# Kernel optimization log

Measured on AMD Instinct MI355X. Metric: run time of the kernel, lower is better.

## Reference

```python
import jax, jax.numpy as jnp
import numpy as np

B, N, C, H = 128, 8732, 512, 19  # batch, priors, channels, feature map side
IMG = 300.0
FG = 19


def setup_inputs() -> dict:
    key = jax.random.key(0)
    ks = jax.random.split(key, 10)
    loc = jax.random.normal(ks[0], (B, N, 4), jnp.float32) * 0.5
    conf = jax.random.normal(ks[1], (B, N, 2), jnp.float32)
    priors = jax.random.uniform(ks[2], (N, 4), jnp.float32, minval=0.05, maxval=0.95)
    features = jax.random.normal(ks[3], (B, C, H, H), jnp.float32)
    w1 = jax.random.normal(ks[4], (C, 4096), jnp.float32) * 0.01
    b1 = jnp.zeros((4096,), jnp.float32)
    w2 = jax.random.normal(ks[5], (4096, 4096), jnp.float32) * 0.01
    b2 = jnp.zeros((4096,), jnp.float32)
    w3 = jax.random.normal(ks[6], (4096, FG), jnp.float32) * 0.01
    b3 = jnp.zeros((FG,), jnp.float32)
    return {"loc": loc, "conf": conf, "priors": priors, "features": features,
            "w1": w1, "b1": b1, "w2": w2, "b2": b2, "w3": w3, "b3": b3}


def _decode(loc, priors):
    # SSD decode, variances=[0.1, 0.2]; priors are (cx, cy, w, h)
    cxcy = priors[:, :2] + loc[..., :2] * 0.1 * priors[:, 2:]
    wh = priors[:, 2:] * jnp.exp(loc[..., 2:] * 0.2)
    xy1 = cxcy - 0.5 * wh
    return jnp.concatenate([xy1, xy1 + wh], axis=-1)  # [B,N,4] corner form


def _best_prior(loc, conf, priors):
    boxes = _decode(loc, priors)                       # [B,N,4]
    probs = jax.nn.softmax(conf, axis=-1)              # [B,N,2]
    car = jnp.argmax(probs, axis=-1) == 1              # [B,N] argmax class == car
    score = jnp.where(car, probs[..., 1], -jnp.inf)
    best = jnp.argmax(score, axis=-1)                  # [B]
    best_box = jnp.take_along_axis(boxes, best[:, None, None], axis=1)[:, 0]  # [B,4]
    has_car = jnp.any(car, axis=-1)                    # [B]
    geom = (best_box[:, 2] > best_box[:, 0]) & (best_box[:, 3] > best_box[:, 1])
    valid = has_car & geom
    result = jnp.where(has_car[:, None], best_box, 0.0)
    result = jnp.clip(result, 0.0, 1.0)
    return result, valid


def _extract(features, boxes, valid):
    # per-box crop + global max pool -> [B,C], zero for invalid boxes
    ceil_num = features.shape[2]
    step = IMG / ceil_num
    b = jnp.clip(boxes * IMG, 0.0, IMG) / step
    b = jnp.floor(jnp.clip(b, 0.0, ceil_num - 1.0)).astype(jnp.int32)  # [B,4]=x1,y1,x2,y2
    r = jnp.arange(ceil_num)
    mh = (r[None, :] >= b[:, 1:2]) & (r[None, :] <= b[:, 3:4])  # [B,H] rows
    mw = (r[None, :] >= b[:, 0:1]) & (r[None, :] <= b[:, 2:3])  # [B,W] cols
    mask = mh[:, None, :, None] & mw[:, None, None, :]          # [B,1,H,W]
    m = jnp.max(jnp.where(mask, features, -jnp.inf), axis=(2, 3))  # [B,C]
    return jnp.where(valid[:, None], m, 0.0)


def reference(loc, conf, priors, features, w1, b1, w2, b2, w3, b3):
    boxes, valid = _best_prior(loc, conf, priors)
    feat = _extract(features, boxes, valid)             # [B,512]
    h = jax.nn.relu(feat @ w1 + b1)
    h = jax.nn.relu(h @ w2 + b2)
    fg_cls = h @ w3 + b3                                # [B,19]
    return fg_cls, boxes, valid.astype(jnp.int32)
```

## Files before the change

### kernel.cpp

```cpp
#include <hip/hip_runtime.h>
#include <math.h>

#define BATCH 128
#define NPRI  8732
#define CCH   512
#define HH    19
#define NHID  4096
#define FGC   19

typedef unsigned short u16;
typedef __attribute__((ext_vector_type(8))) short bf16x8;
typedef __attribute__((ext_vector_type(4))) float f32x4;

__device__ __forceinline__ u16 f2bf(float f) {
  unsigned u = __float_as_uint(f);
  u += 0x7fff + ((u >> 16) & 1);
  return (u16)(u >> 16);
}

__global__ void k_best(const float* __restrict__ conf,
                       const float* __restrict__ loc,
                       const float* __restrict__ priors,
                       float* __restrict__ out_boxes,
                       float* __restrict__ out_valid,
                       int4* __restrict__ crop, int* __restrict__ vflag) {
  int b = blockIdx.x;
  int t = threadIdx.x;
  const float4* cb = (const float4*)(conf + (size_t)b * NPRI * 2);
  float bd = -INFINITY; int bn = 0x7fffffff;
  for (int j = t; j < NPRI / 2; j += 256) {
    float4 v = cb[j];
    float d0 = v.y - v.x, d1 = v.w - v.z;
    if (d0 > bd) { bd = d0; bn = 2 * j; }
    if (d1 > bd) { bd = d1; bn = 2 * j + 1; }
  }
  __shared__ float ls[256]; __shared__ int li[256];
  ls[t] = bd; li[t] = bn;
  __syncthreads();
  for (int off = 128; off > 0; off >>= 1) {
    if (t < off) {
      float s2 = ls[t + off]; int n2 = li[t + off];
      if (s2 > ls[t] || (s2 == ls[t] && n2 < li[t])) { ls[t] = s2; li[t] = n2; }
    }
    __syncthreads();
  }
  if (t == 0) {
    float bdf = ls[0]; int bnf = li[0];
    bool hc = bdf > 0.0f;
    float r0 = 0.f, r1 = 0.f, r2 = 0.f, r3 = 0.f;
    bool valid = false;
    if (hc) {
      const float* lp = loc + ((size_t)b * NPRI + bnf) * 4;
      const float* pp = priors + (size_t)bnf * 4;
      float l0 = lp[0], l1 = lp[1], l2 = lp[2], l3 = lp[3];
      float pcx = pp[0], pcy = pp[1], pw = pp[2], ph = pp[3];
      float cx = pcx + (l0 * 0.1f) * pw;
      float cy = pcy + (l1 * 0.1f) * ph;
      float w = pw * expf(l2 * 0.2f);
      float h = ph * expf(l3 * 0.2f);
      float x1 = cx - 0.5f * w, y1 = cy - 0.5f * h;
      float x2 = x1 + w, y2 = y1 + h;
      valid = (x2 > x1) && (y2 > y1);
      r0 = fminf(fmaxf(x1, 0.f), 1.f);
      r1 = fminf(fmaxf(y1, 0.f), 1.f);
      r2 = fminf(fmaxf(x2, 0.f), 1.f);
      r3 = fminf(fmaxf(y2, 0.f), 1.f);
    }
    out_boxes[b * 4 + 0] = r0; out_boxes[b * 4 + 1] = r1;
    out_boxes[b * 4 + 2] = r2; out_boxes[b * 4 + 3] = r3;
    out_valid[b] = valid ? 1.0f : 0.0f;
    const float stepF = (float)(300.0 / 19.0);
    float q0 = fminf(fmaxf(r0 * 300.0f, 0.0f), 300.0f) / stepF;
    float q1 = fminf(fmaxf(r1 * 300.0f, 0.0f), 300.0f) / stepF;
    float q2 = fminf(fmaxf(r2 * 300.0f, 0.0f), 300.0f) / stepF;
    float q3 = fminf(fmaxf(r3 * 300.0f, 0.0f), 300.0f) / stepF;
    int ix1 = (int)floorf(fminf(fmaxf(q0, 0.0f), 18.0f));
    int iy1 = (int)floorf(fminf(fmaxf(q1, 0.0f), 18.0f));
    int ix2 = (int)floorf(fminf(fmaxf(q2, 0.0f), 18.0f));
    int iy2 = (int)floorf(fminf(fmaxf(q3, 0.0f), 18.0f));
    crop[b] = make_int4(ix1, iy1, ix2, iy2);
    vflag[b] = valid ? 1 : 0;
  }
}

__global__ void k_extract(const float* __restrict__ fin,
                          const int4* __restrict__ crop,
                          const int* __restrict__ vflag,
                          u16* __restrict__ feat) {
  int blk = blockIdx.x;
  int b = blk >> 7;
  int tile = blk & 127;
  int wave = threadIdx.x >> 6;
  int lane = threadIdx.x & 63;
  int c = tile * 4 + wave;
  if (!vflag[b]) {
    if (lane == 0) feat[b * CCH + c] = 0;
    return;
  }
  int4 cr = crop[b];
  const float* p = fin + (size_t)(b * CCH + c) * (HH * HH);
  float m = -INFINITY;
  #pragma unroll
  for (int it = 0; it < 6; it++) {
    int idx = it * 64 + lane;
    if (idx < HH * HH) {
      int yy = idx / HH, xx = idx - yy * HH;
      bool in = (yy >= cr.y) & (yy <= cr.w) & (xx >= cr.x) & (xx <= cr.z);
      float v = p[idx];
      if (in) m = fmaxf(m, v);
    }
  }
  #pragma unroll
  for (int off = 32; off > 0; off >>= 1) m = fmaxf(m, __shfl_xor(m, off));
  if (lane == 0) feat[b * CCH + c] = f2bf(m);
}

__global__ __launch_bounds__(256) void k_gemm1(const u16* __restrict__ A,
                                               const float* __restrict__ W,
                                               const float* __restrict__ bias,
                                               u16* __restrict__ H1) {
  const int N = NHID, K = CCH;
  int nb = blockIdx.x;
  int t = threadIdx.x;
  int lane = t & 63, wave = t >> 6;
  int q = lane >> 4, r = lane & 15;
  int wm = (wave & 1) * 64, wn = (wave >> 1) * 32;
  int n0 = nb * 64;

  __shared__ u16 As[128 * 40];
  __shared__ u16 Bs[64 * 40];

  f32x4 acc[4][2];
  #pragma unroll
  for (int i = 0; i < 4; i++)
    #pragma unroll
    for (int j = 0; j < 2; j++) {
      acc[i][j].x = 0.f; acc[i][j].y = 0.f; acc[i][j].z = 0.f; acc[i][j].w = 0.f;
    }

  int am = t >> 1, ah = (t & 1) * 16;
  int kp = t >> 4;
  int n4 = (t & 15) * 4;

  for (int k0 = 0; k0 < K; k0 += 32) {
    const u16* asrc = A + (size_t)am * K + k0 + ah;
    uint4 a0 = *(const uint4*)asrc;
    uint4 a1 = *(const uint4*)(asrc + 8);
    const float* wsrc = W + (size_t)(k0 + 2 * kp) * N + n0 + n4;
    float4 w0 = *(const float4*)wsrc;
    float4 w1v = *(const float4*)(wsrc + N);
    __syncthreads();
    *(uint4*)&As[am * 40 + ah]     = a0;
    *(uint4*)&As[am * 40 + ah + 8] = a1;
    {
      unsigned pk0 = (unsigned)f2bf(w0.x) | ((unsigned)f2bf(w1v.x) << 16);
      unsigned pk1 = (unsigned)f2bf(w0.y) | ((unsigned)f2bf(w1v.y) << 16);
      unsigned pk2 = (unsigned)f2bf(w0.z) | ((unsigned)f2bf(w1v.z) << 16);
      unsigned pk3 = (unsigned)f2bf(w0.w) | ((unsigned)f2bf(w1v.w) << 16);
      *(unsigned*)&Bs[(n4 + 0) * 40 + 2 * kp] = pk0;
      *(unsigned*)&Bs[(n4 + 1) * 40 + 2 * kp] = pk1;
      *(unsigned*)&Bs[(n4 + 2) * 40 + 2 * kp] = pk2;
      *(unsigned*)&Bs[(n4 + 3) * 40 + 2 * kp] = pk3;
    }
    __syncthreads();
    bf16x8 af[4], bfr[2];
    #pragma unroll
    for (int i = 0; i < 4; i++)
      af[i] = *(const bf16x8*)&As[(wm + 16 * i + r) * 40 + q * 8];
    #pragma unroll
    for (int j = 0; j < 2; j++)
      bfr[j] = *(const bf16x8*)&Bs[(wn + 16 * j + r) * 40 + q * 8];
    #pragma unroll
    for (int i = 0; i < 4; i++)
      #pragma unroll
      for (int j = 0; j < 2; j++)
        acc[i][j] = __builtin_amdgcn_mfma_f32_16x16x32_bf16(af[i], bfr[j],
                                                            acc[i][j], 0, 0, 0);
  }

  #pragma unroll
  for (int j = 0; j < 2; j++) {
    int col = n0 + wn + 16 * j + r;
    float bv = bias[col];
    #pragma unroll
    for (int i = 0; i < 4; i++) {
      #pragma unroll
      for (int reg = 0; reg < 4; reg++) {
        int row = wm + 16 * i + q * 4 + reg;
        float v = fmaxf(acc[i][j][reg] + bv, 0.0f);
        H1[(size_t)row * N + col] = f2bf(v);
      }
    }
  }
}

template <int KSPL>
__global__ __launch_bounds__(256) void k_mfma(const u16* __restrict__ A,
                                              const float* __restrict__ W,
                                              float* __restrict__ part, int K) {
  const int N = NHID;
  int nb = blockIdx.x;
  int ks = blockIdx.y;
  int Kper = K / KSPL;
  int k0b = ks * Kper;
  int t = threadIdx.x;
  int lane = t & 63, wave = t >> 6;
  int q = lane >> 4, r = lane & 15;

  __shared__ u16 As[128 * 40];
  __shared__ u16 Bs[64 * 40];

  int wm = (wave & 1) * 64;
  int wn = (wave >> 1) * 32;
  int n0 = nb * 64;

  f32x4 acc[4][2];
  #pragma unroll
  for (int i = 0; i < 4; i++)
    #pragma unroll
    for (int j = 0; j < 2; j++) {
      acc[i][j].x = 0.f; acc[i][j].y = 0.f; acc[i][j].z = 0.f; acc[i][j].w = 0.f;
    }

  int am = t >> 1, ah = (t & 1) * 16;
  int kp = t >> 4;
  int n4 = (t & 15) * 4;

  for (int k0 = k0b; k0 < k0b + Kper; k0 += 32) {
    const u16* asrc = A + (size_t)am * K + k0 + ah;
    uint4 a0 = *(const uint4*)asrc;
    uint4 a1 = *(const uint4*)(asrc + 8);
    const float* wsrc = W + (size_t)(k0 + 2 * kp) * N + n0 + n4;
    float4 w0 = *(const float4*)wsrc;
    float4 w1v = *(const float4*)(wsrc + N);
    __syncthreads();
    *(uint4*)&As[am * 40 + ah]     = a0;
    *(uint4*)&As[am * 40 + ah + 8] = a1;
    {
      unsigned pk0 = (unsigned)f2bf(w0.x) | ((unsigned)f2bf(w1v.x) << 16);
      unsigned pk1 = (unsigned)f2bf(w0.y) | ((unsigned)f2bf(w1v.y) << 16);
      unsigned pk2 = (unsigned)f2bf(w0.z) | ((unsigned)f2bf(w1v.z) << 16);
      unsigned pk3 = (unsigned)f2bf(w0.w) | ((unsigned)f2bf(w1v.w) << 16);
      *(unsigned*)&Bs[(n4 + 0) * 40 + 2 * kp] = pk0;
      *(unsigned*)&Bs[(n4 + 1) * 40 + 2 * kp] = pk1;
      *(unsigned*)&Bs[(n4 + 2) * 40 + 2 * kp] = pk2;
      *(unsigned*)&Bs[(n4 + 3) * 40 + 2 * kp] = pk3;
    }
    __syncthreads();
    bf16x8 af[4], bfr[2];
    #pragma unroll
    for (int i = 0; i < 4; i++)
      af[i] = *(const bf16x8*)&As[(wm + 16 * i + r) * 40 + q * 8];
    #pragma unroll
    for (int j = 0; j < 2; j++)
      bfr[j] = *(const bf16x8*)&Bs[(wn + 16 * j + r) * 40 + q * 8];
    #pragma unroll
    for (int i = 0; i < 4; i++)
      #pragma unroll
      for (int j = 0; j < 2; j++)
        acc[i][j] = __builtin_amdgcn_mfma_f32_16x16x32_bf16(af[i], bfr[j],
                                                            acc[i][j], 0, 0, 0);
  }

  float* dst = part + (size_t)ks * (BATCH * NHID);
  #pragma unroll
  for (int i = 0; i < 4; i++)
    #pragma unroll
    for (int j = 0; j < 2; j++) {
      int col = n0 + wn + 16 * j + r;
      #pragma unroll
      for (int reg = 0; reg < 4; reg++) {
        int row = wm + 16 * i + q * 4 + reg;
        dst[(size_t)row * N + col] = acc[i][j][reg];
      }
    }
}

template <int KSPL>
__global__ void k_finalize(const float* __restrict__ part,
                           const float* __restrict__ bias,
                           float* __restrict__ outf) {
  int idx = (blockIdx.x * 256 + threadIdx.x) * 4;
  float4 s = *(const float4*)(part + idx);
  #pragma unroll
  for (int p = 1; p < KSPL; p++) {
    float4 v = *(const float4*)(part + (size_t)p * (BATCH * NHID) + idx);
    s.x += v.x; s.y += v.y; s.z += v.z; s.w += v.w;
  }
  float4 bv = *(const float4*)(bias + (idx & (NHID - 1)));
  s.x = fmaxf(s.x + bv.x, 0.0f); s.y = fmaxf(s.y + bv.y, 0.0f);
  s.z = fmaxf(s.z + bv.z, 0.0f); s.w = fmaxf(s.w + bv.w, 0.0f);
  *(float4*)(outf + idx) = s;
}

__global__ void k_gemm3p(const float* __restrict__ h2,
                         const float* __restrict__ w3,
                         float* __restrict__ part3) {
  int kc = blockIdx.x;
  int t = threadIdx.x;
  __shared__ float wl[32 * FGC];
  for (int i = t; i < 32 * FGC; i += 128) wl[i] = w3[kc * 32 * FGC + i];
  __syncthreads();
  const float* hp = h2 + (size_t)t * NHID + kc * 32;
  float acc[FGC];
  #pragma unroll
  for (int j = 0; j < FGC; j++) acc[j] = 0.0f;
  for (int k = 0; k < 32; k++) {
    float hv = hp[k];
    const float* wp = &wl[k * FGC];
    #pragma unroll
    for (int j = 0; j < FGC; j++) acc[j] += hv * wp[j];
  }
  float* dst = part3 + (size_t)kc * (BATCH * FGC) + t * FGC;
  #pragma unroll
  for (int j = 0; j < FGC; j++) dst[j] = acc[j];
}

__global__ void k_fin3(const float* __restrict__ part3,
                       const float* __restrict__ b3,
                       float* __restrict__ out) {
  int j = blockIdx.x * 256 + threadIdx.x;
  if (j >= BATCH * FGC) return;
  float s = 0.0f;
  for (int p = 0; p < 128; p++) s += part3[(size_t)p * (BATCH * FGC) + j];
  out[j] = s + b3[j % FGC];
}

extern "C" void kernel_launch(void* const* d_in, const int* in_sizes, int n_in,
                              void* d_out, int out_size, void* d_ws, size_t ws_size,
                              hipStream_t stream) {
  const float* loc      = (const float*)d_in[0];
  const float* conf     = (const float*)d_in[1];
  const float* priors   = (const float*)d_in[2];
  const float* features = (const float*)d_in[3];
  const float* w1 = (const float*)d_in[4];
  const float* b1 = (const float*)d_in[5];
  const float* w2 = (const float*)d_in[6];
  const float* b2 = (const float*)d_in[7];
  const float* w3 = (const float*)d_in[8];
  const float* b3 = (const float*)d_in[9];
  float* out = (float*)d_out;

  char* ws = (char*)d_ws;
  float* part  = (float*)ws;
  float* part3 = (float*)(ws + (size_t)16 * 1024 * 1024);
  float* h2    = (float*)(ws + (size_t)18 * 1024 * 1024);
  u16*   featb = (u16*)(ws + (size_t)20 * 1024 * 1024);
  u16*   h1b   = (u16*)(ws + (size_t)20 * 1024 * 1024 + 256 * 1024);
  int4*  crop  = (int4*)(ws + (size_t)21 * 1024 * 1024 + 512 * 1024);
  int*   vfl   = (int*)(crop + BATCH);

  k_best<<<BATCH, 256, 0, stream>>>(conf, loc, priors,
                                    out + BATCH * FGC,
                                    out + BATCH * FGC + BATCH * 4, crop, vfl);
  k_extract<<<BATCH * (CCH / 4), 256, 0, stream>>>(features, crop, vfl, featb);
  k_gemm1<<<64, 256, 0, stream>>>(featb, w1, b1, h1b);
  k_mfma<8><<<dim3(64, 8), 256, 0, stream>>>(h1b, w2, part, NHID);
  k_finalize<8><<<512, 256, 0, stream>>>(part, b2, h2);
  k_gemm3p<<<128, 128, 0, stream>>>(h2, w3, part3);
  k_fin3<<<10, 256, 0, stream>>>(part3, b3, out);
}
```

Measured before the change: 275.1 us.

## Split-K first GEMM, fuse layer-2 finalize into layer-3, crop-only extract loop

```diff
diff --git a/kernel.cpp b/kernel.cpp
--- a/kernel.cpp
+++ b/kernel.cpp
@@ -1,4 +1,5 @@
 #include <hip/hip_runtime.h>
+#include <hip/hip_bf16.h>
 #include <math.h>
 
 #define BATCH 128
@@ -98,100 +99,18 @@
     return;
   }
   int4 cr = crop[b];
+  int wcnt = cr.z - cr.x + 1;
+  int cnt = wcnt * (cr.w - cr.y + 1);
   const float* p = fin + (size_t)(b * CCH + c) * (HH * HH);
   float m = -INFINITY;
-  #pragma unroll
-  for (int it = 0; it < 6; it++) {
-    int idx = it * 64 + lane;
-    if (idx < HH * HH) {
-      int yy = idx / HH, xx = idx - yy * HH;
-      bool in = (yy >= cr.y) & (yy <= cr.w) & (xx >= cr.x) & (xx <= cr.z);
-      float v = p[idx];
-      if (in) m = fmaxf(m, v);
-    }
+  for (int i = lane; i < cnt; i += 64) {
+    int yy = cr.y + i / wcnt;
+    int xx = cr.x + i % wcnt;
+    m = fmaxf(m, p[yy * HH + xx]);
   }
   #pragma unroll
   for (int off = 32; off > 0; off >>= 1) m = fmaxf(m, __shfl_xor(m, off));
   if (lane == 0) feat[b * CCH + c] = f2bf(m);
-}
-
-__global__ __launch_bounds__(256) void k_gemm1(const u16* __restrict__ A,
-                                               const float* __restrict__ W,
-                                               const float* __restrict__ bias,
-                                               u16* __restrict__ H1) {
-  const int N = NHID, K = CCH;
-  int nb = blockIdx.x;
-  int t = threadIdx.x;
-  int lane = t & 63, wave = t >> 6;
-  int q = lane >> 4, r = lane & 15;
-  int wm = (wave & 1) * 64, wn = (wave >> 1) * 32;
-  int n0 = nb * 64;
-
-  __shared__ u16 As[128 * 40];
-  __shared__ u16 Bs[64 * 40];
-
-  f32x4 acc[4][2];
-  #pragma unroll
-  for (int i = 0; i < 4; i++)
-    #pragma unroll
-    for (int j = 0; j < 2; j++) {
-      acc[i][j].x = 0.f; acc[i][j].y = 0.f; acc[i][j].z = 0.f; acc[i][j].w = 0.f;
-    }
-
-  int am = t >> 1, ah = (t & 1) * 16;
-  int kp = t >> 4;
-  int n4 = (t & 15) * 4;
-
-  for (int k0 = 0; k0 < K; k0 += 32) {
-    const u16* asrc = A + (size_t)am * K + k0 + ah;
-    uint4 a0 = *(const uint4*)asrc;
-    uint4 a1 = *(const uint4*)(asrc + 8);
-    const float* wsrc = W + (size_t)(k0 + 2 * kp) * N + n0 + n4;
-    float4 w0 = *(const float4*)wsrc;
-    float4 w1v = *(const float4*)(wsrc + N);
-    __syncthreads();
-    *(uint4*)&As[am * 40 + ah]     = a0;
-    *(uint4*)&As[am * 40 + ah + 8] = a1;
-    {
-      unsigned pk0 = (unsigned)f2bf(w0.x) | ((unsigned)f2bf(w1v.x) << 16);
-      unsigned pk1 = (unsigned)f2bf(w0.y) | ((unsigned)f2bf(w1v.y) << 16);
-      unsigned pk2 = (unsigned)f2bf(w0.z) | ((unsigned)f2bf(w1v.z) << 16);
-      unsigned pk3 = (unsigned)f2bf(w0.w) | ((unsigned)f2bf(w1v.w) << 16);
-      *(unsigned*)&Bs[(n4 + 0) * 40 + 2 * kp] = pk0;
-      *(unsigned*)&Bs[(n4 + 1) * 40 + 2 * kp] = pk1;
-      *(unsigned*)&Bs[(n4 + 2) * 40 + 2 * kp] = pk2;
-      *(unsigned*)&Bs[(n4 + 3) * 40 + 2 * kp] = pk3;
-    }
-    __syncthreads();
-    bf16x8 af[4], bfr[2];
-    #pragma unroll
-    for (int i = 0; i < 4; i++)
-      af[i] = *(const bf16x8*)&As[(wm + 16 * i + r) * 40 + q * 8];
-    #pragma unroll
-    for (int j = 0; j < 2; j++)
-      bfr[j] = *(const bf16x8*)&Bs[(wn + 16 * j + r) * 40 + q * 8];
-    #pragma unroll
-    for (int i = 0; i < 4; i++)
-      #pragma unroll
-      for (int j = 0; j < 2; j++)
-        acc[i][j] = __builtin_amdgcn_mfma_f32_16x16x32_bf16(af[i], bfr[j],
-                                                            acc[i][j], 0, 0, 0);
-  }
-
-  #pragma unroll
-  for (int j = 0; j < 2; j++) {
-    int col = n0 + wn + 16 * j + r;
-    float bv = bias[col];
-    #pragma unroll
-    for (int i = 0; i < 4; i++) {
-      #pragma unroll
-      for (int reg = 0; reg < 4; reg++) {
-        int row = wm + 16 * i + q * 4 + reg;
-        float v = fmaxf(acc[i][j][reg] + bv, 0.0f);
-        H1[(size_t)row * N + col] = f2bf(v);
-      }
-    }
-  }
 }
 
 template <int KSPL>
@@ -237,14 +156,14 @@
     *(uint4*)&As[am * 40 + ah]     = a0;
     *(uint4*)&As[am * 40 + ah + 8] = a1;
     {
-      unsigned pk0 = (unsigned)f2bf(w0.x) | ((unsigned)f2bf(w1v.x) << 16);
-      unsigned pk1 = (unsigned)f2bf(w0.y) | ((unsigned)f2bf(w1v.y) << 16);
-      unsigned pk2 = (unsigned)f2bf(w0.z) | ((unsigned)f2bf(w1v.z) << 16);
-      unsigned pk3 = (unsigned)f2bf(w0.w) | ((unsigned)f2bf(w1v.w) << 16);
-      *(unsigned*)&Bs[(n4 + 0) * 40 + 2 * kp] = pk0;
-      *(unsigned*)&Bs[(n4 + 1) * 40 + 2 * kp] = pk1;
-      *(unsigned*)&Bs[(n4 + 2) * 40 + 2 * kp] = pk2;
-      *(unsigned*)&Bs[(n4 + 3) * 40 + 2 * kp] = pk3;
+      __hip_bfloat162 p0 = __float22bfloat162_rn(make_float2(w0.x, w1v.x));
+      __hip_bfloat162 p1 = __float22bfloat162_rn(make_float2(w0.y, w1v.y));
+      __hip_bfloat162 p2 = __float22bfloat162_rn(make_float2(w0.z, w1v.z));
+      __hip_bfloat162 p3 = __float22bfloat162_rn(make_float2(w0.w, w1v.w));
+      *(__hip_bfloat162*)&Bs[(n4 + 0) * 40 + 2 * kp] = p0;
+      *(__hip_bfloat162*)&Bs[(n4 + 1) * 40 + 2 * kp] = p1;
+      *(__hip_bfloat162*)&Bs[(n4 + 2) * 40 + 2 * kp] = p2;
+      *(__hip_bfloat162*)&Bs[(n4 + 3) * 40 + 2 * kp] = p3;
     }
     __syncthreads();
     bf16x8 af[4], bfr[2];
@@ -277,9 +196,9 @@
 }
 
 template <int KSPL>
-__global__ void k_finalize(const float* __restrict__ part,
-                           const float* __restrict__ bias,
-                           float* __restrict__ outf) {
+__global__ void k_finalize_bf16(const float* __restrict__ part,
+                                const float* __restrict__ bias,
+                                u16* __restrict__ outb) {
   int idx = (blockIdx.x * 256 + threadIdx.x) * 4;
   float4 s = *(const float4*)(part + idx);
   #pragma unroll
@@ -290,21 +209,35 @@
   float4 bv = *(const float4*)(bias + (idx & (NHID - 1)));
   s.x = fmaxf(s.x + bv.x, 0.0f); s.y = fmaxf(s.y + bv.y, 0.0f);
   s.z = fmaxf(s.z + bv.z, 0.0f); s.w = fmaxf(s.w + bv.w, 0.0f);
-  *(float4*)(outf + idx) = s;
-}
-
-__global__ void k_gemm3p(const float* __restrict__ h2,
+  ushort4 o;
+  o.x = f2bf(s.x); o.y = f2bf(s.y); o.z = f2bf(s.z); o.w = f2bf(s.w);
+  *(ushort4*)(outb + idx) = o;
+}
+
+__global__ void k_gemm3p(const float* __restrict__ part,
+                         const float* __restrict__ b2,
                          const float* __restrict__ w3,
                          float* __restrict__ part3) {
   int kc = blockIdx.x;
   int t = threadIdx.x;
   __shared__ float wl[32 * FGC];
+  __shared__ float ht[128 * 33];
   for (int i = t; i < 32 * FGC; i += 128) wl[i] = w3[kc * 32 * FGC + i];
+  int klane = t & 31, mg = t >> 5;
+  float bv = b2[kc * 32 + klane];
+  for (int i = 0; i < 32; i++) {
+    int m = mg * 32 + i;
+    const float* pp = part + (size_t)m * NHID + kc * 32 + klane;
+    float s = pp[0];
+    #pragma unroll
+    for (int p = 1; p < 8; p++) s += pp[(size_t)p * (BATCH * NHID)];
+    ht[m * 33 + klane] = fmaxf(s + bv, 0.0f);
+  }
   __syncthreads();
-  const float* hp = h2 + (size_t)t * NHID + kc * 32;
   float acc[FGC];
   #pragma unroll
   for (int j = 0; j < FGC; j++) acc[j] = 0.0f;
+  const float* hp = &ht[t * 33];
   for (int k = 0; k < 32; k++) {
     float hv = hp[k];
     const float* wp = &wl[k * FGC];
@@ -344,7 +277,6 @@
   char* ws = (char*)d_ws;
   float* part  = (float*)ws;
   float* part3 = (float*)(ws + (size_t)16 * 1024 * 1024);
-  float* h2    = (float*)(ws + (size_t)18 * 1024 * 1024);
   u16*   featb = (u16*)(ws + (size_t)20 * 1024 * 1024);
   u16*   h1b   = (u16*)(ws + (size_t)20 * 1024 * 1024 + 256 * 1024);
   int4*  crop  = (int4*)(ws + (size_t)21 * 1024 * 1024 + 512 * 1024);
@@ -354,9 +286,9 @@
                                     out + BATCH * FGC,
                                     out + BATCH * FGC + BATCH * 4, crop, vfl);
   k_extract<<<BATCH * (CCH / 4), 256, 0, stream>>>(features, crop, vfl, featb);
-  k_gemm1<<<64, 256, 0, stream>>>(featb, w1, b1, h1b);
+  k_mfma<4><<<dim3(64, 4), 256, 0, stream>>>(featb, w1, part, CCH);
+  k_finalize_bf16<4><<<512, 256, 0, stream>>>(part, b1, h1b);
   k_mfma<8><<<dim3(64, 8), 256, 0, stream>>>(h1b, w2, part, NHID);
-  k_finalize<8><<<512, 256, 0, stream>>>(part, b2, h2);
-  k_gemm3p<<<128, 128, 0, stream>>>(h2, w3, part3);
+  k_gemm3p<<<128, 128, 0, stream>>>(part, b2, w3, part3);
   k_fin3<<<10, 256, 0, stream>>>(part3, b3, out);
 }
```

Result: faster. 261.1 us (median of 2 runs) (-5.1%).
